# Kernel tuning notes

Measured on AMD Instinct MI355X. Metric: run time of the kernel, lower is better.

Reference implementation:

```python
import jax, jax.numpy as jnp
import numpy as np
import math

B, SEQ, E, H, NB, NHYP = 4, 1024, 512, 8, 64, 6
V, HID, NC, ENC = 32000, 2048, 6, 6
DH = E // H


def _pos_encoding(n, e, dtype):
    pos = jnp.arange(n, dtype=dtype)[:, None]
    div = jnp.exp(-jnp.arange(0, e, 2, dtype=dtype) * (math.log(10000.0) / e))
    ang = pos * div  # [n, e/2]
    pe = jnp.zeros((n, e), dtype)
    pe = pe.at[:, 0::2].set(jnp.sin(ang))
    pe = pe.at[:, 1::2].set(jnp.cos(ang))
    return pe


def _layer_norm(x, g, b):
    m = x.mean(-1, keepdims=True)
    v = ((x - m) ** 2).mean(-1, keepdims=True)
    return (x - m) / jnp.sqrt(v + 1e-5) * g + b


def _lsh_attention(x, Wq, bq, Wv, bv, hyper):
    b, n, e = x.shape
    q = x @ Wq + bq
    v = x @ Wv + bv
    q4 = q.reshape(b, n, H, DH)  # [b,n,h,d]
    v4 = v.reshape(b, n, H, DH)
    # bucket hashing: append bias 1, project on hyperplanes, binarize, binary-encode
    aug = jnp.concatenate([q4, jnp.ones((b, n, H, 1), q.dtype)], axis=-1)
    proj = jnp.einsum('bnhe,ey->bnhy', aug, hyper)
    bits = (proj >= 0).astype(q.dtype)
    pows = (2 ** jnp.arange(NHYP)).astype(q.dtype)
    buckets = jnp.einsum('bnhy,y->bnh', bits, pows).astype(jnp.int32)
    bh = buckets.transpose(0, 2, 1)  # [b,h,n]
    qh = q4.transpose(0, 2, 1, 3)  # [b,h,n,d]
    vh = v4.transpose(0, 2, 1, 3)
    scores = jnp.einsum('bhnd,bhmd->bhnm', qh, qh) / math.sqrt(e)
    # torch code zeroes q rows at their OWN bucket and sums q_c @ q_c^T over all
    # NB buckets; that equals scores * (NB - 2 + [bucket_i == bucket_j]) exactly.
    same = bh[:, :, :, None] == bh[:, :, None, :]
    count = (NB - 2 + same.astype(jnp.int32)).astype(scores.dtype)
    attn = jax.nn.softmax(scores * count, axis=-1)
    out = jnp.einsum('bhnm,bhmd->bhnd', attn, vh)
    return out.transpose(0, 2, 1, 3).reshape(b, n, e)


def setup_inputs() -> dict:
    key = jax.random.key(0)
    ks = jax.random.split(key, 16)
    s = 0.02
    emb = jax.random.normal(ks[0], (V, E), jnp.float32) * s
    emb = emb.at[V - 1].set(0.0)  # padding_idx row
    return dict(
        inputs=jax.random.randint(ks[1], (B, SEQ), 0, V),
        emb=emb,
        gamma=jnp.ones((E,), jnp.float32),
        beta=jnp.zeros((E,), jnp.float32),
        Wq=jax.random.normal(ks[2], (E, E), jnp.float32) * s,
        bq=jnp.zeros((E,), jnp.float32),
        Wv=jax.random.normal(ks[3], (E, E), jnp.float32) * s,
        bv=jnp.zeros((E,), jnp.float32),
        hyper=jax.random.normal(ks[4], (DH + 1, NHYP), jnp.float32),
        W1=jax.random.normal(ks[5], (E, HID), jnp.float32) * s,
        b1=jnp.zeros((HID,), jnp.float32),
        W2=jax.random.normal(ks[6], (HID, E), jnp.float32) * s,
        b2=jnp.zeros((E,), jnp.float32),
        Wm=jax.random.normal(ks[7], (E * SEQ, NC), jnp.float32) * 0.002,
        bm=jnp.zeros((NC,), jnp.float32),
    )


def reference(inputs, emb, gamma, beta, Wq, bq, Wv, bv, hyper, W1, b1, W2, b2, Wm, bm):
    x = emb[inputs]  # [B, SEQ, E]
    x = x + _pos_encoding(x.shape[1], x.shape[2], x.dtype)
    for _ in range(ENC):  # shared weights across encoders
        a = _lsh_attention(x, Wq, bq, Wv, bv, hyper)
        x = _layer_norm(a, gamma, beta)
        x = jax.nn.relu(x @ W1 + b1) @ W2 + b2 + x
        x = _layer_norm(x, gamma, beta)
    x = x.reshape(x.shape[0], -1)
    return x @ Wm + bm  # [B, NC]
```

## Files before the change

kernel.cpp:

```cpp
#include <hip/hip_runtime.h>
#include <hip/hip_bf16.h>
#include <math.h>

#define B_    4
#define SEQ_  1024
#define E_    512
#define H_    8
#define DH_   64
#define NHYP_ 6
#define HID_  2048
#define NC_   6
#define ENC_  6
#define BH_   (B_*H_)

typedef __attribute__((ext_vector_type(8))) short short8;
typedef __attribute__((ext_vector_type(4))) float f32x4;

static __device__ __forceinline__ float wave_rsum(float v){
#pragma unroll
  for(int o=32;o;o>>=1) v += __shfl_down(v,o,64);
  return v;
}
static __device__ __forceinline__ ushort f2b(float v){
  __hip_bfloat16 h = __float2bfloat16(v);
  return *(ushort*)&h;
}
static __device__ __forceinline__ void gload16(const void* g, void* l){
  __builtin_amdgcn_global_load_lds(
      (const __attribute__((address_space(1))) void*)g,
      (__attribute__((address_space(3))) void*)l,
      16, 0, 0);
}

__global__ void embed_pe_kernel(const int* __restrict__ inp, const float* __restrict__ emb,
                                float* __restrict__ x, ushort* __restrict__ xh){
  int row = blockIdx.x;
  int s = row & (SEQ_-1);
  int idx = inp[row];
  const float* er = emb + (size_t)idx*E_;
  float* xr = x + (size_t)row*E_;
  ushort* hr = xh + (size_t)row*E_;
  for(int c=threadIdx.x;c<E_;c+=blockDim.x){
    int i = c>>1;
    float div = expf(-(float)i * 0.0359778920780319646f);
    float ang = (float)s * div;
    float pe = (c&1) ? cosf(ang) : sinf(ang);
    float v = er[c] + pe;
    xr[c] = v;
    hr[c] = f2b(v);
  }
}

__global__ __launch_bounds__(256) void transpose_cast(
    const float* __restrict__ W, ushort* __restrict__ Wt, int K, int N){
  __shared__ float T[32][33];
  int tx = threadIdx.x & 31, ty = threadIdx.x >> 5;
  int n0 = blockIdx.x*32, k0 = blockIdx.y*32;
#pragma unroll
  for(int i=0;i<32;i+=8) T[ty+i][tx] = W[(size_t)(k0+ty+i)*N + n0+tx];
  __syncthreads();
#pragma unroll
  for(int i=0;i<32;i+=8)
    Wt[(size_t)(n0+ty+i)*K + k0+tx] = f2b(T[tx][ty+i]);
}

__global__ void concat_bias(const float* __restrict__ a, const float* __restrict__ b,
                            float* __restrict__ o){
  int t = threadIdx.x + blockIdx.x*256;
  if(t < 512) o[t] = a[t];
  else if(t < 1024) o[t] = b[t-512];
}

template<int BM, int BN, int EPI>
__global__ __launch_bounds__(256) void gemm_mfma(
    const ushort* __restrict__ A, const ushort* __restrict__ Bt,
    const float* __restrict__ bias, const float* __restrict__ res,
    void* __restrict__ C0, void* __restrict__ C1, void* __restrict__ C2,
    int M, int N, int K)
{
  constexpr int MI = BM/32, NI = BN/32;
  constexpr int ACH = BM/32, BCH = BN/32;
  __shared__ ushort As[2][BM*64];
  __shared__ ushort Bs[2][BN*64];
  int tid = threadIdx.x;
  int w = tid>>6, lane = tid&63, g = lane>>4, li = lane&15;
  int wr = w>>1, wc = w&1;
  int bm = blockIdx.y*BM, bn = blockIdx.x*BN;
  int NK = K>>6;

  f32x4 acc[MI][NI] = {};

  auto issue = [&](int ks, int pb){
    int k0 = ks*64;
#pragma unroll
    for(int it=0; it<ACH; ++it){
      int c = it*256 + tid; int r = c>>3; int kq = ((c&7)^(r&7))*8;
      gload16(&A[(size_t)(bm+r)*K + k0 + kq], &As[pb][it*2048 + w*512]);
    }
#pragma unroll
    for(int it=0; it<BCH; ++it){
      int c = it*256 + tid; int r = c>>3; int kq = ((c&7)^(r&7))*8;
      gload16(&Bt[(size_t)(bn+r)*K + k0 + kq], &Bs[pb][it*2048 + w*512]);
    }
  };

  issue(0, 0);
  __syncthreads();
  for(int ks=0; ks<NK; ++ks){
    if(ks+1 < NK) issue(ks+1, (ks+1)&1);
    int pb = ks&1;
#pragma unroll
    for(int kc=0; kc<2; ++kc){
      short8 af[MI], bf[NI];
#pragma unroll
      for(int mi=0;mi<MI;++mi)
        af[mi] = *(const short8*)&As[pb][(wr*(BM/2)+mi*16+li)*64 + (((kc*4+g)^(li&7))*8)];
#pragma unroll
      for(int ni=0;ni<NI;++ni)
        bf[ni] = *(const short8*)&Bs[pb][(wc*(BN/2)+ni*16+li)*64 + (((kc*4+g)^(li&7))*8)];
#pragma unroll
      for(int mi=0;mi<MI;++mi)
#pragma unroll
        for(int ni=0;ni<NI;++ni)
          acc[mi][ni] = __builtin_amdgcn_mfma_f32_16x16x32_bf16(af[mi], bf[ni], acc[mi][ni], 0,0,0);
    }
    __syncthreads();
  }

#pragma unroll
  for(int mi=0;mi<MI;++mi){
    int rbase = bm + wr*(BM/2) + mi*16 + g*4;
#pragma unroll
    for(int ni=0;ni<NI;++ni){
      int cc = bn + wc*(BN/2) + ni*16 + li;
      float bv = bias[cc];
      float vv[4];
#pragma unroll
      for(int j=0;j<4;++j) vv[j] = acc[mi][ni][j] + bv;
      if(EPI==0){
#pragma unroll
        for(int j=0;j<4;++j) ((float*)C0)[(size_t)(rbase+j)*N + cc] = vv[j];
      } else if(EPI==1){
#pragma unroll
        for(int j=0;j<4;++j) ((ushort*)C0)[(size_t)(rbase+j)*N + cc] = f2b(fmaxf(vv[j],0.0f));
      } else if(EPI==2){
#pragma unroll
        for(int j=0;j<4;++j){
          size_t o = (size_t)(rbase+j)*N + cc;
          ((float*)C0)[o] = vv[j] + res[o];
        }
      } else {
        if(cc < 512){
          int h = cc>>6, d = cc&63;
#pragma unroll
          for(int j=0;j<4;++j){
            int r = rbase + j;
            ((float*)C0)[(size_t)r*512 + cc] = vv[j];
            int b = r>>10, n = r&1023;
            ((ushort*)C1)[(((size_t)(b*8+h))*1024 + n)*64 + d] = f2b(vv[j]);
          }
        } else {
          int cl = cc - 512; int h = cl>>6, d = cl&63;
          int b = rbase>>10, n = rbase&1023;
          ushort4 pk;
          pk.x = f2b(vv[0]); pk.y = f2b(vv[1]); pk.z = f2b(vv[2]); pk.w = f2b(vv[3]);
          *(ushort4*)&((ushort*)C2)[(((size_t)(b*8+h))*64 + d)*1024 + n] = pk;
        }
      }
    }
  }
}

__global__ void bucket_kernel(const float* __restrict__ q, const float* __restrict__ hyper,
                              int* __restrict__ buckets, float* __restrict__ qn2){
  int t = blockIdx.x*256 + threadIdx.x;
  if(t >= B_*SEQ_*H_) return;
  int h = t & (H_-1);
  int n = (t >> 3) & (SEQ_-1);
  int b = t >> 13;
  const float* qr = q + ((size_t)(b*SEQ_ + n))*E_ + h*DH_;
  float pr[NHYP_];
#pragma unroll
  for(int y=0;y<NHYP_;++y) pr[y] = hyper[DH_*NHYP_ + y];
  float s2 = 0.f;
  for(int d=0;d<DH_;++d){
    float qd = qr[d];
    s2 += qd*qd;
#pragma unroll
    for(int y=0;y<NHYP_;++y) pr[y] += qd * hyper[d*NHYP_ + y];
  }
  int bk = 0;
#pragma unroll
  for(int y=0;y<NHYP_;++y) bk |= (pr[y] >= 0.0f) ? (1<<y) : 0;
  int o = (b*H_ + h)*SEQ_ + n;
  buckets[o] = bk;
  qn2[o] = s2;
}

__global__ __launch_bounds__(256) void attn_mfma_kernel(
    const ushort* __restrict__ Qh,
    const ushort* __restrict__ Vt,
    const int* __restrict__ buckets,
    const float* __restrict__ qn2,
    float* __restrict__ outp)
{
  int bid = blockIdx.x;
  int bh = bid & 31;
  int qt = bid >> 5;
  int b = bh >> 3, h = bh & 7;
  int tid = threadIdx.x;
  int w = tid >> 6, lane = tid & 63;
  int g = lane >> 4, li = lane & 15;

  __shared__ ushort Ks[2][64*64];
  __shared__ ushort Vs[2][64*64];
  __shared__ ushort Ps[64*68];
  __shared__ int bks[2][64];
  __shared__ int bqs[64];
  __shared__ float mred[4];

  const ushort* Qbase = Qh + (size_t)bh*SEQ_*DH_;
  const ushort* Vbase = Vt + (size_t)bh*DH_*SEQ_;
  const int* Bb = buckets + bh*SEQ_;
  const float* qn = qn2 + bh*SEQ_;
  int q0 = qt*64;

  auto issue = [&](int kt, int pb){
    int j0 = kt*64;
#pragma unroll
    for(int it=0; it<2; ++it){
      int c = it*256 + tid; int r = c>>3; int ks = ((c&7)^(r&7))*8;
      gload16(&Qbase[(size_t)(j0+r)*DH_ + ks], &Ks[pb][it*2048 + w*512]);
      gload16(&Vbase[(size_t)r*SEQ_ + j0 + ks], &Vs[pb][it*2048 + w*512]);
    }
    if(tid < 16) gload16(&Bb[j0 + tid*4], &bks[pb][0]);
  };

  issue(0, 0);
  short8 qa[2];
  int qrow = q0 + w*16 + li;
#pragma unroll
  for(int kc=0; kc<2; ++kc)
    qa[kc] = *(const short8*)&Qbase[(size_t)qrow*DH_ + kc*32 + g*8];
  if(tid < 64) bqs[tid] = Bb[q0 + tid];

  float mx = 0.f;
  for(int i=tid;i<SEQ_;i+=256) mx = fmaxf(mx, qn[i]);
#pragma unroll
  for(int o=32;o;o>>=1) mx = fmaxf(mx, __shfl_xor(mx, o, 64));
  if(lane==0) mred[w] = mx;
  __syncthreads();
  float maxn = sqrtf(fmaxf(fmaxf(mred[0],mred[1]), fmaxf(mred[2],mred[3])));

  const float invsq = 0.04419417382415922f;
  const float c63 = invsq * 63.0f;
  float Mrow[4];
#pragma unroll
  for(int i=0;i<4;++i)
    Mrow[i] = c63 * sqrtf(qn[q0 + w*16 + g*4 + i]) * maxn + 1.0f;

  f32x4 acc_o[4] = {};
  float psum[4] = {0.f,0.f,0.f,0.f};

  for(int kt=0; kt<16; ++kt){
    if(kt < 15) issue(kt+1, (kt+1)&1);
    int pb = kt&1;

    f32x4 accs[4];
    __builtin_amdgcn_s_setprio(1);
#pragma unroll
    for(int nt=0; nt<4; ++nt){
      f32x4 z = {};
#pragma unroll
      for(int kc=0; kc<2; ++kc){
        short8 kb = *(const short8*)&Ks[pb][(nt*16+li)*64 + (((kc*4+g)^(li&7))*8)];
        z = __builtin_amdgcn_mfma_f32_16x16x32_bf16(qa[kc], kb, z, 0,0,0);
      }
      accs[nt] = z;
    }
    __builtin_amdgcn_s_setprio(0);
    int bkc[4];
#pragma unroll
    for(int nt=0;nt<4;++nt) bkc[nt] = bks[pb][nt*16 + li];

#pragma unroll
    for(int i=0;i<4;++i){
      int rloc = w*16 + g*4 + i;
      int bq = bqs[rloc];
      float rs = 0.f;
#pragma unroll
      for(int nt=0;nt<4;++nt){
        float cnt = (bkc[nt] == bq) ? 63.f : 62.f;
        float e = __expf(accs[nt][i] * (invsq * cnt) - Mrow[i]);
        rs += e;
        Ps[rloc*68 + nt*16 + li] = f2b(e);
      }
      psum[i] += rs;
    }
    __builtin_amdgcn_s_setprio(1);
#pragma unroll
    for(int dt=0; dt<4; ++dt){
      f32x4 z = acc_o[dt];
#pragma unroll
      for(int kc=0; kc<2; ++kc){
        short8 pa = *(const short8*)&Ps[(w*16+li)*68 + kc*32 + g*8];
        short8 vb = *(const short8*)&Vs[pb][(dt*16+li)*64 + (((kc*4+g)^(li&7))*8)];
        z = __builtin_amdgcn_mfma_f32_16x16x32_bf16(pa, vb, z, 0,0,0);
      }
      acc_o[dt] = z;
    }
    __builtin_amdgcn_s_setprio(0);
    __syncthreads();
  }
#pragma unroll
  for(int i=0;i<4;++i){
#pragma unroll
    for(int o=8;o;o>>=1) psum[i] += __shfl_xor(psum[i], o, 64);
  }
  float* obase = outp + ((size_t)(b*SEQ_ + q0 + w*16 + g*4))*E_ + h*DH_;
#pragma unroll
  for(int i=0;i<4;++i){
    float inv = 1.0f / fmaxf(psum[i], 1e-35f);
#pragma unroll
    for(int dt=0;dt<4;++dt)
      obase[(size_t)i*E_ + dt*16 + li] = acc_o[dt][i] * inv;
  }
}

__global__ __launch_bounds__(256) void ln_kernel(
    const float* __restrict__ in, const float* __restrict__ g,
    const float* __restrict__ bb, float* __restrict__ outp,
    ushort* __restrict__ oh){
  int row = blockIdx.x*4 + (threadIdx.x>>6);
  int lane = threadIdx.x & 63;
  const float4* xr = (const float4*)(in + (size_t)row*E_);
  float4 v0 = xr[lane*2], v1 = xr[lane*2+1];
  float s  = v0.x+v0.y+v0.z+v0.w + v1.x+v1.y+v1.z+v1.w;
  float s2 = v0.x*v0.x+v0.y*v0.y+v0.z*v0.z+v0.w*v0.w
           + v1.x*v1.x+v1.y*v1.y+v1.z*v1.z+v1.w*v1.w;
#pragma unroll
  for(int o=32;o;o>>=1){ s += __shfl_xor(s,o,64); s2 += __shfl_xor(s2,o,64); }
  float mean = s*(1.0f/E_);
  float var  = s2*(1.0f/E_) - mean*mean;
  float inv = rsqrtf(var + 1e-5f);
  const float4* g4 = (const float4*)(g) + lane*2;
  const float4* b4 = (const float4*)(bb) + lane*2;
  float4 g0 = g4[0], g1 = g4[1], b0 = b4[0], b1 = b4[1];
  float4 y0, y1;
  y0.x=(v0.x-mean)*inv*g0.x+b0.x; y0.y=(v0.y-mean)*inv*g0.y+b0.y;
  y0.z=(v0.z-mean)*inv*g0.z+b0.z; y0.w=(v0.w-mean)*inv*g0.w+b0.w;
  y1.x=(v1.x-mean)*inv*g1.x+b1.x; y1.y=(v1.y-mean)*inv*g1.y+b1.y;
  y1.z=(v1.z-mean)*inv*g1.z+b1.z; y1.w=(v1.w-mean)*inv*g1.w+b1.w;
  float4* orow = (float4*)(outp + (size_t)row*E_) + lane*2;
  orow[0] = y0; orow[1] = y1;
  ushort hs[8];
  hs[0]=f2b(y0.x); hs[1]=f2b(y0.y); hs[2]=f2b(y0.z); hs[3]=f2b(y0.w);
  hs[4]=f2b(y1.x); hs[5]=f2b(y1.y); hs[6]=f2b(y1.z); hs[7]=f2b(y1.w);
  *(uint4*)&oh[(size_t)row*E_ + lane*8] = *(uint4*)hs;
}

__global__ void final_partial(const float* __restrict__ x, const float* __restrict__ Wm,
                              float* __restrict__ part){
  int b  = blockIdx.x >> 7;
  int ch = blockIdx.x & 127;
  const float* xb = x + (size_t)b*SEQ_*E_;
  int k0 = ch*4096;
  float acc[NC_] = {};
  for(int k=k0+threadIdx.x; k<k0+4096; k+=256){
    float xv = xb[k];
    const float* wrow = Wm + (size_t)k*NC_;
#pragma unroll
    for(int c=0;c<NC_;++c) acc[c] += xv*wrow[c];
  }
#pragma unroll
  for(int c=0;c<NC_;++c) acc[c] = wave_rsum(acc[c]);
  __shared__ float r[4][NC_];
  int w = threadIdx.x>>6, lane = threadIdx.x&63;
  if(lane==0){
#pragma unroll
    for(int c=0;c<NC_;++c) r[w][c] = acc[c];
  }
  __syncthreads();
  if(threadIdx.x==0){
#pragma unroll
    for(int c=0;c<NC_;++c)
      part[(size_t)blockIdx.x*NC_ + c] = r[0][c]+r[1][c]+r[2][c]+r[3][c];
  }
}

__global__ void final_reduce(const float* __restrict__ part, const float* __restrict__ bm,
                             float* __restrict__ out){
  int t = threadIdx.x;
  if(t >= B_*NC_) return;
  int b = t / NC_, c = t % NC_;
  float s = bm[c];
  for(int i=0;i<128;++i) s += part[(size_t)(b*128+i)*NC_ + c];
  out[t] = s;
}

extern "C" void kernel_launch(void* const* d_in, const int* in_sizes, int n_in,
                              void* d_out, int out_size, void* d_ws, size_t ws_size,
                              hipStream_t stream){
  const int*   inp   = (const int*)d_in[0];
  const float* emb   = (const float*)d_in[1];
  const float* gamma = (const float*)d_in[2];
  const float* beta  = (const float*)d_in[3];
  const float* Wq    = (const float*)d_in[4];
  const float* bq    = (const float*)d_in[5];
  const float* Wv    = (const float*)d_in[6];
  const float* bv    = (const float*)d_in[7];
  const float* hyper = (const float*)d_in[8];
  const float* W1    = (const float*)d_in[9];
  const float* b1    = (const float*)d_in[10];
  const float* W2    = (const float*)d_in[11];
  const float* b2    = (const float*)d_in[12];
  const float* Wm    = (const float*)d_in[13];
  const float* bm    = (const float*)d_in[14];
  float* out = (float*)d_out;

  char* ws = (char*)d_ws;
  size_t off = 0;
  auto alloc = [&](size_t bytes)->void*{
    void* p = ws + off; off += (bytes + 255) & ~(size_t)255; return p;
  };
  const size_t NTOK = (size_t)B_*SEQ_;
  float*  X    = (float*)alloc(NTOK*E_*sizeof(float));
  float*  Q    = (float*)alloc(NTOK*E_*sizeof(float));
  float*  A    = (float*)alloc(NTOK*E_*sizeof(float));
  ushort* Xh   = (ushort*)alloc(NTOK*E_*sizeof(ushort));
  ushort* Hh   = (ushort*)alloc(NTOK*HID_*sizeof(ushort));
  int*    Bk   = (int*)  alloc((size_t)BH_*SEQ_*sizeof(int));
  float*  Qn2  = (float*)alloc((size_t)BH_*SEQ_*sizeof(float));
  float*  Pp   = (float*)alloc((size_t)B_*128*NC_*sizeof(float));
  ushort* Qh   = (ushort*)alloc((size_t)BH_*SEQ_*DH_*sizeof(ushort));
  ushort* Vt   = (ushort*)alloc((size_t)BH_*DH_*SEQ_*sizeof(ushort));
  ushort* WqvT = (ushort*)alloc((size_t)1024*E_*sizeof(ushort));
  ushort* W1T  = (ushort*)alloc((size_t)HID_*E_*sizeof(ushort));
  ushort* W2T  = (ushort*)alloc((size_t)E_*HID_*sizeof(ushort));
  float*  bqv  = (float*)alloc(1024*sizeof(float));
  (void)ws_size; (void)in_sizes; (void)n_in; (void)out_size;

  transpose_cast<<<dim3(E_/32,  E_/32),  256, 0, stream>>>(Wq, WqvT, E_, E_);
  transpose_cast<<<dim3(E_/32,  E_/32),  256, 0, stream>>>(Wv, WqvT + (size_t)512*E_, E_, E_);
  transpose_cast<<<dim3(HID_/32,E_/32),  256, 0, stream>>>(W1, W1T, E_, HID_);
  transpose_cast<<<dim3(E_/32,  HID_/32),256, 0, stream>>>(W2, W2T, HID_, E_);
  concat_bias<<<4, 256, 0, stream>>>(bq, bv, bqv);

  embed_pe_kernel<<<B_*SEQ_, 256, 0, stream>>>(inp, emb, X, Xh);

  dim3 gQV(1024/64,  (B_*SEQ_)/64);
  dim3 gF1(HID_/128, (B_*SEQ_)/128);
  dim3 gF2(E_/64,    (B_*SEQ_)/64);
  for(int l=0;l<ENC_;++l){
    gemm_mfma<64,64,5><<<gQV, 256, 0, stream>>>(Xh, WqvT, bqv, nullptr, Q, Qh, Vt, B_*SEQ_, 1024, E_);
    bucket_kernel<<<(B_*SEQ_*H_)/256, 256, 0, stream>>>(Q, hyper, Bk, Qn2);
    attn_mfma_kernel<<<BH_*16, 256, 0, stream>>>(Qh, Vt, Bk, Qn2, A);
    ln_kernel<<<B_*SEQ_/4, 256, 0, stream>>>(A, gamma, beta, X, Xh);
    gemm_mfma<128,128,1><<<gF1, 256, 0, stream>>>(Xh, W1T, b1, nullptr, Hh, nullptr, nullptr, B_*SEQ_, HID_, E_);
    gemm_mfma<64,64,2><<<gF2, 256, 0, stream>>>(Hh, W2T, b2, X, A, nullptr, nullptr, B_*SEQ_, E_, HID_);
    ln_kernel<<<B_*SEQ_/4, 256, 0, stream>>>(A, gamma, beta, X, Xh);
  }
  final_partial<<<B_*128, 256, 0, stream>>>(X, Wm, Pp);
  final_reduce<<<1, 32, 0, stream>>>(Pp, bm, out);
}
```

Measured before the change: 599.4 us.

## Fold LSH hyperplane projection into QV GEMM and drop fp32 Q output

Precomputes Wq·hyper (and the matching bias) as 48 extra output columns of the QV GEMM, so the bucket projections come straight out of the GEMM and the fp32 Q buffer no longer has to be written or re-read. A lighter encode kernel now reads the bf16 Qh for the norms and the projected values for the bucket bits. The QV and FFN2 GEMMs also move to 128-row tiles. Computing the projections from a folded bf16 weight instead of fp32 q can flip bucket bits for values near zero, and the grid with 1088 columns spends extra work on padded columns.

```diff
diff --git a/kernel.cpp b/kernel.cpp
--- a/kernel.cpp
+++ b/kernel.cpp
@@ -12,6 +12,7 @@
 #define NC_   6
 #define ENC_  6
 #define BH_   (B_*H_)
+#define NCAT_ 1088
 
 typedef __attribute__((ext_vector_type(8))) short short8;
 typedef __attribute__((ext_vector_type(4))) float f32x4;
@@ -24,6 +25,10 @@
 static __device__ __forceinline__ ushort f2b(float v){
   __hip_bfloat16 h = __float2bfloat16(v);
   return *(ushort*)&h;
+}
+static __device__ __forceinline__ float b2f(ushort u){
+  unsigned int x = ((unsigned int)u) << 16;
+  return *(float*)&x;
 }
 static __device__ __forceinline__ void gload16(const void* g, void* l){
   __builtin_amdgcn_global_load_lds(
@@ -64,11 +69,33 @@
     Wt[(size_t)(n0+ty+i)*K + k0+tx] = f2b(T[tx][ty+i]);
 }
 
-__global__ void concat_bias(const float* __restrict__ a, const float* __restrict__ b,
-                            float* __restrict__ o){
-  int t = threadIdx.x + blockIdx.x*256;
-  if(t < 512) o[t] = a[t];
-  else if(t < 1024) o[t] = b[t-512];
+__global__ void wproj_build(const float* __restrict__ Wq, const float* __restrict__ hyper,
+                            ushort* __restrict__ WcatT){
+  int t = blockIdx.x*256 + threadIdx.x;
+  int c = t >> 9, k = t & 511;
+  float s = 0.f;
+  if(c < 48){
+    int h = c/6, y = c%6;
+    const float* wr = Wq + (size_t)k*E_ + h*DH_;
+    for(int d=0;d<DH_;++d) s += wr[d]*hyper[d*NHYP_+y];
+  }
+  WcatT[(size_t)(1024+c)*E_ + k] = f2b(s);
+}
+
+__global__ void bias_build(const float* __restrict__ bq, const float* __restrict__ bv,
+                           const float* __restrict__ hyper, float* __restrict__ bcat){
+  int t = blockIdx.x*256 + threadIdx.x;
+  if(t >= NCAT_) return;
+  float v;
+  if(t < 512) v = bq[t];
+  else if(t < 1024) v = bv[t-512];
+  else if(t < 1072){
+    int c = t - 1024, h = c/6, y = c%6;
+    float s = hyper[DH_*NHYP_ + y];
+    for(int d=0;d<DH_;++d) s += bq[h*DH_+d]*hyper[d*NHYP_+y];
+    v = s;
+  } else v = 0.f;
+  bcat[t] = v;
 }
 
 template<int BM, int BN, int EPI>
@@ -155,46 +182,49 @@
 #pragma unroll
           for(int j=0;j<4;++j){
             int r = rbase + j;
-            ((float*)C0)[(size_t)r*512 + cc] = vv[j];
             int b = r>>10, n = r&1023;
             ((ushort*)C1)[(((size_t)(b*8+h))*1024 + n)*64 + d] = f2b(vv[j]);
           }
-        } else {
+        } else if(cc < 1024){
           int cl = cc - 512; int h = cl>>6, d = cl&63;
           int b = rbase>>10, n = rbase&1023;
           ushort4 pk;
           pk.x = f2b(vv[0]); pk.y = f2b(vv[1]); pk.z = f2b(vv[2]); pk.w = f2b(vv[3]);
           *(ushort4*)&((ushort*)C2)[(((size_t)(b*8+h))*64 + d)*1024 + n] = pk;
+        } else if(cc < 1072){
+#pragma unroll
+          for(int j=0;j<4;++j)
+            ((float*)C0)[(size_t)(rbase+j)*64 + (cc-1024)] = vv[j];
         }
       }
     }
   }
 }
 
-__global__ void bucket_kernel(const float* __restrict__ q, const float* __restrict__ hyper,
-                              int* __restrict__ buckets, float* __restrict__ qn2){
+__global__ __launch_bounds__(256) void encode_kernel(
+    const ushort* __restrict__ Qh, const float* __restrict__ Pr,
+    int* __restrict__ buckets, float* __restrict__ qn2){
   int t = blockIdx.x*256 + threadIdx.x;
-  if(t >= B_*SEQ_*H_) return;
-  int h = t & (H_-1);
-  int n = (t >> 3) & (SEQ_-1);
-  int b = t >> 13;
-  const float* qr = q + ((size_t)(b*SEQ_ + n))*E_ + h*DH_;
-  float pr[NHYP_];
-#pragma unroll
-  for(int y=0;y<NHYP_;++y) pr[y] = hyper[DH_*NHYP_ + y];
+  int h = t & 7, row = t >> 3;
+  int b = row >> 10, n = row & 1023;
+  int bhn = (b*8+h)*1024 + n;
+  const short8* qp = (const short8*)&Qh[(size_t)bhn*DH_];
   float s2 = 0.f;
-  for(int d=0;d<DH_;++d){
-    float qd = qr[d];
-    s2 += qd*qd;
-#pragma unroll
-    for(int y=0;y<NHYP_;++y) pr[y] += qd * hyper[d*NHYP_ + y];
-  }
+#pragma unroll
+  for(int c=0;c<8;++c){
+    short8 v = qp[c];
+#pragma unroll
+    for(int j=0;j<8;++j){
+      float f = b2f((ushort)v[j]);
+      s2 += f*f;
+    }
+  }
+  qn2[bhn] = s2;
+  const float* pr = Pr + (size_t)row*64 + h*NHYP_;
   int bk = 0;
 #pragma unroll
   for(int y=0;y<NHYP_;++y) bk |= (pr[y] >= 0.0f) ? (1<<y) : 0;
-  int o = (b*H_ + h)*SEQ_ + n;
-  buckets[o] = bk;
-  qn2[o] = s2;
+  buckets[bhn] = bk;
 }
 
 __global__ __launch_bounds__(256) void attn_mfma_kernel(
@@ -425,8 +455,8 @@
   };
   const size_t NTOK = (size_t)B_*SEQ_;
   float*  X    = (float*)alloc(NTOK*E_*sizeof(float));
-  float*  Q    = (float*)alloc(NTOK*E_*sizeof(float));
   float*  A    = (float*)alloc(NTOK*E_*sizeof(float));
+  float*  Pr   = (float*)alloc(NTOK*64*sizeof(float));
   ushort* Xh   = (ushort*)alloc(NTOK*E_*sizeof(ushort));
   ushort* Hh   = (ushort*)alloc(NTOK*HID_*sizeof(ushort));
   int*    Bk   = (int*)  alloc((size_t)BH_*SEQ_*sizeof(int));
@@ -434,30 +464,31 @@
   float*  Pp   = (float*)alloc((size_t)B_*128*NC_*sizeof(float));
   ushort* Qh   = (ushort*)alloc((size_t)BH_*SEQ_*DH_*sizeof(ushort));
   ushort* Vt   = (ushort*)alloc((size_t)BH_*DH_*SEQ_*sizeof(ushort));
-  ushort* WqvT = (ushort*)alloc((size_t)1024*E_*sizeof(ushort));
+  ushort* WcatT= (ushort*)alloc((size_t)NCAT_*E_*sizeof(ushort));
   ushort* W1T  = (ushort*)alloc((size_t)HID_*E_*sizeof(ushort));
   ushort* W2T  = (ushort*)alloc((size_t)E_*HID_*sizeof(ushort));
-  float*  bqv  = (float*)alloc(1024*sizeof(float));
+  float*  bcat = (float*)alloc(NCAT_*sizeof(float));
   (void)ws_size; (void)in_sizes; (void)n_in; (void)out_size;
 
-  transpose_cast<<<dim3(E_/32,  E_/32),  256, 0, stream>>>(Wq, WqvT, E_, E_);
-  transpose_cast<<<dim3(E_/32,  E_/32),  256, 0, stream>>>(Wv, WqvT + (size_t)512*E_, E_, E_);
+  transpose_cast<<<dim3(E_/32,  E_/32),  256, 0, stream>>>(Wq, WcatT, E_, E_);
+  transpose_cast<<<dim3(E_/32,  E_/32),  256, 0, stream>>>(Wv, WcatT + (size_t)512*E_, E_, E_);
+  wproj_build<<<128, 256, 0, stream>>>(Wq, hyper, WcatT);
   transpose_cast<<<dim3(HID_/32,E_/32),  256, 0, stream>>>(W1, W1T, E_, HID_);
   transpose_cast<<<dim3(E_/32,  HID_/32),256, 0, stream>>>(W2, W2T, HID_, E_);
-  concat_bias<<<4, 256, 0, stream>>>(bq, bv, bqv);
+  bias_build<<<5, 256, 0, stream>>>(bq, bv, hyper, bcat);
 
   embed_pe_kernel<<<B_*SEQ_, 256, 0, stream>>>(inp, emb, X, Xh);
 
-  dim3 gQV(1024/64,  (B_*SEQ_)/64);
+  dim3 gQV(NCAT_/64, (B_*SEQ_)/128);
   dim3 gF1(HID_/128, (B_*SEQ_)/128);
-  dim3 gF2(E_/64,    (B_*SEQ_)/64);
+  dim3 gF2(E_/64,    (B_*SEQ_)/128);
   for(int l=0;l<ENC_;++l){
-    gemm_mfma<64,64,5><<<gQV, 256, 0, stream>>>(Xh, WqvT, bqv, nullptr, Q, Qh, Vt, B_*SEQ_, 1024, E_);
-    bucket_kernel<<<(B_*SEQ_*H_)/256, 256, 0, stream>>>(Q, hyper, Bk, Qn2);
+    gemm_mfma<128,64,5><<<gQV, 256, 0, stream>>>(Xh, WcatT, bcat, nullptr, Pr, Qh, Vt, B_*SEQ_, NCAT_, E_);
+    encode_kernel<<<(B_*SEQ_*H_)/256, 256, 0, stream>>>(Qh, Pr, Bk, Qn2);
     attn_mfma_kernel<<<BH_*16, 256, 0, stream>>>(Qh, Vt, Bk, Qn2, A);
     ln_kernel<<<B_*SEQ_/4, 256, 0, stream>>>(A, gamma, beta, X, Xh);
     gemm_mfma<128,128,1><<<gF1, 256, 0, stream>>>(Xh, W1T, b1, nullptr, Hh, nullptr, nullptr, B_*SEQ_, HID_, E_);
-    gemm_mfma<64,64,2><<<gF2, 256, 0, stream>>>(Hh, W2T, b2, X, A, nullptr, nullptr, B_*SEQ_, E_, HID_);
+    gemm_mfma<128,64,2><<<gF2, 256, 0, stream>>>(Hh, W2T, b2, X, A, nullptr, nullptr, B_*SEQ_, E_, HID_);
     ln_kernel<<<B_*SEQ_/4, 256, 0, stream>>>(A, gamma, beta, X, Xh);
   }
   final_partial<<<B_*128, 256, 0, stream>>>(X, Wm, Pp);
```

After: 650.5 us. 1.09x slower.
